# Performance work log

Measured on AMD Instinct MI355X. Metric: run time of the kernel, lower is better.

The kernel has to match this reference:

```python
import jax, jax.numpy as jnp
import numpy as np

MAX_ORDERS = 8
HIDDEN = 128
B, P = 64, 1024
FREQ_SCALE = 500.0  # Hz range for synthetic peaks
TOL = 2.0           # harmonic match tolerance from source


def setup_inputs() -> dict:
    key = jax.random.key(0)
    ks = jax.random.split(key, 6)
    peak_frequencies = jax.random.uniform(ks[0], (B, P), dtype=jnp.float32) * FREQ_SCALE
    peak_magnitudes = jax.random.normal(ks[1], (B, P), dtype=jnp.float32)
    def lin(k, fan_in, fan_out):
        return jax.random.normal(k, (fan_in, fan_out), dtype=jnp.float32) * (1.0 / np.sqrt(fan_in))
    W1 = lin(ks[2], 2, HIDDEN);        b1 = jnp.zeros((HIDDEN,), jnp.float32)
    W2 = lin(ks[3], HIDDEN, HIDDEN);   b2 = jnp.zeros((HIDDEN,), jnp.float32)
    W3 = lin(ks[4], HIDDEN, MAX_ORDERS); b3 = jnp.zeros((MAX_ORDERS,), jnp.float32)
    return {"peak_frequencies": peak_frequencies, "peak_magnitudes": peak_magnitudes,
            "W1": W1, "b1": b1, "W2": W2, "b2": b2, "W3": W3, "b3": b3}


def _fundamental_freq(freqs, mags):
    """Vectorized form of the triple-nested harmonic-matching loop.
    Returns the fundamental frequency of the LAST batch element, faithfully
    reproducing the original code (which overwrites fundamental_freq per batch)."""
    valid = mags > 0.0                                   # (B,P)
    # matched[b,i,j] = exists order in [2, max_orders] with |f_j - f_i*order| < TOL
    matched = jnp.zeros(freqs.shape[:1] + (freqs.shape[1], freqs.shape[1]), dtype=bool)
    for order in range(2, MAX_ORDERS + 1):
        matched = matched | (jnp.abs(freqs[:, None, :] - freqs[:, :, None] * order) < TOL)
    eye = jnp.eye(freqs.shape[1], dtype=bool)[None]      # exclude j == i
    harmonics = jnp.sum(matched & valid[:, None, :] & ~eye, axis=2)  # (B,P) int counts
    cand = valid & (harmonics > 0)                       # candidate peaks
    any_cand = jnp.any(cand, axis=1)                     # (B,)
    # lexicographic max over (harmonics, magnitude); argmax breaks ties by first index,
    # matching Python's stable sort over i-ascending candidate lists.
    h_masked = jnp.where(cand, harmonics, -1)
    max_h = jnp.max(h_masked, axis=1, keepdims=True)
    best = cand & (h_masked == max_h)
    mag_masked = jnp.where(best, mags, -jnp.inf)
    idx_cand = jnp.argmax(mag_masked, axis=1)
    idx_fallback = jnp.argmax(mags, axis=1)
    idx = jnp.where(any_cand, idx_cand, idx_fallback)    # (B,)
    fund = jnp.take_along_axis(freqs, idx[:, None], axis=1)[:, 0]
    return fund[-1]


def reference(peak_frequencies, peak_magnitudes, W1, b1, W2, b2, W3, b3):
    # peak_detector MLP (eval mode: dropout is identity)
    x = jnp.stack([peak_frequencies, peak_magnitudes], axis=-1)   # (B,P,2)
    h = jax.nn.relu(x @ W1 + b1)
    h = jax.nn.relu(h @ W2 + b2)
    order_probs = h @ W3 + b3                                     # (B,P,max_orders)
    fundamental_freq = _fundamental_freq(peak_frequencies, peak_magnitudes)
    return (order_probs, fundamental_freq)
```

## Files before the change

### kernel.cpp

```cpp
#include <hip/hip_runtime.h>
#include <hip/hip_bf16.h>

#define HID   128
#define PNUM  1024
#define LASTB 63
#define BP    (64 * PNUM)
#define NBLK  512
#define PPB   128
#define H2S   132

typedef __attribute__((ext_vector_type(8))) short short8;
typedef __attribute__((ext_vector_type(4))) float f32x4;

__device__ __forceinline__ unsigned pk2(float a, float b) {
    __hip_bfloat162 h = __float22bfloat162_rn(make_float2(a, b));
    union { __hip_bfloat162 h2; unsigned u; } c;
    c.h2 = h;
    return c.u;
}
__device__ __forceinline__ unsigned long long umax64(unsigned long long a,
                                                     unsigned long long b) {
    return a > b ? a : b;
}

__global__ __launch_bounds__(256) void fusedA(
    const float* __restrict__ freqs, const float* __restrict__ mags,
    const float* __restrict__ W1, const float* __restrict__ b1,
    const float* __restrict__ W2, const float* __restrict__ b2,
    const float* __restrict__ W3, const float* __restrict__ b3,
    float* __restrict__ out, unsigned long long* __restrict__ ckArr,
    unsigned long long* __restrict__ fkW)
{
    __shared__ unsigned short sW2T[HID * HID];
    __shared__ unsigned short sW3T[16 * HID];
    __shared__ float sH2[4][16 * H2S];
    __shared__ float sf[PNUM], sm[PNUM];
    __shared__ unsigned long long sfb[256];
    __shared__ unsigned long long sKey[2];
    __shared__ int sRed[4];

    const int t = threadIdx.x;
    const int b = blockIdx.x;

    {
        const float4* fb4 = reinterpret_cast<const float4*>(freqs + (size_t)LASTB * PNUM);
        const float4* mb4 = reinterpret_cast<const float4*>(mags  + (size_t)LASTB * PNUM);
        reinterpret_cast<float4*>(sf)[t] = fb4[t];
        reinterpret_cast<float4*>(sm)[t] = mb4[t];
    }

    {
        const int n    = t & 127;
        const int half = t >> 7;
#pragma unroll
        for (int r = 0; r < 8; ++r) {
            const int c  = r * 2 + half;
            const int k0 = c * 8;
            float v[8];
#pragma unroll
            for (int j = 0; j < 8; ++j) v[j] = W2[(k0 + j) * HID + n];
            union { short8 s; unsigned u[4]; } pk;
            pk.u[0] = pk2(v[0], v[1]); pk.u[1] = pk2(v[2], v[3]);
            pk.u[2] = pk2(v[4], v[5]); pk.u[3] = pk2(v[6], v[7]);
            *(short8*)&sW2T[n * HID + (c ^ (n & 15)) * 8] = pk.s;
        }
    }
    {
        const int o = t >> 4;
        const int c = t & 15;
        union { short8 s; unsigned u[4]; } pk;
        if (o < 8) {
            float v[8];
#pragma unroll
            for (int j = 0; j < 8; ++j) v[j] = W3[(c * 8 + j) * 8 + o];
            pk.u[0] = pk2(v[0], v[1]); pk.u[1] = pk2(v[2], v[3]);
            pk.u[2] = pk2(v[4], v[5]); pk.u[3] = pk2(v[6], v[7]);
        } else {
            pk.u[0] = pk.u[1] = pk.u[2] = pk.u[3] = 0u;
        }
        *(short8*)&sW3T[o * HID + (c ^ (o & 15)) * 8] = pk.s;
    }
    __syncthreads();

    {
        const int i_loc = t >> 7;
        const int jc    = t & 127;
        const int i     = b * 2 + i_loc;
        const float fi  = sf[i];
        float fo[7];
#pragma unroll
        for (int o = 0; o < 7; ++o) fo[o] = __fmul_rn(fi, (float)(o + 2));

        int c = 0;
#pragma unroll
        for (int jj = 0; jj < 8; ++jj) {
            const int j = jj * 128 + jc;
            const float fj = sf[j];
            bool match = false;
#pragma unroll
            for (int o = 0; o < 7; ++o)
                match = match || (fabsf(__fsub_rn(fj, fo[o])) < 2.0f);
            if (match && (sm[j] > 0.0f) && (j != i)) ++c;
        }
#pragma unroll
        for (int off = 32; off > 0; off >>= 1) c += __shfl_down(c, off, 64);
        if ((t & 63) == 0) sRed[t >> 6] = c;
    }
    __syncthreads();

    if ((t & 127) == 0) {
        const int i = b * 2 + (t >> 7);
        const int h = sRed[(t >> 6)] + sRed[(t >> 6) + 1];
        const float mi = sm[i];
        unsigned long long key = 0ull;
        if (mi > 0.0f && h > 0)
            key = ((unsigned long long)h << 42) |
                  ((unsigned long long)__float_as_uint(mi) << 10) |
                  (unsigned long long)(1023 - i);
        sKey[t >> 7] = key;
    }
    __syncthreads();
    if (t == 0) ckArr[b] = umax64(sKey[0], sKey[1]);

    if (b == 0) {
        unsigned long long fk = 0ull;
#pragma unroll
        for (int r = 0; r < 4; ++r) {
            const int i2 = t + 256 * r;
            const unsigned mb = __float_as_uint(sm[i2]);
            const unsigned mo = (mb & 0x80000000u) ? ~mb : (mb | 0x80000000u);
            fk = umax64(fk, ((unsigned long long)mo << 10) |
                            (unsigned long long)(1023 - i2));
        }
        sfb[t] = fk;
        __syncthreads();
        for (int s = 128; s > 0; s >>= 1) {
            if (t < s) sfb[t] = umax64(sfb[t], sfb[t + s]);
            __syncthreads();
        }
        if (t == 0) *fkW = sfb[0];
    }

    const int w    = t >> 6;
    const int lane = t & 63;
    const int cc   = lane & 15;
    const int q    = lane >> 4;
    const int pb   = b * PPB + w * 32;

    const int p0 = pb + cc;
    const int p1 = pb + 16 + cc;
    const float f0 = freqs[p0], m0 = mags[p0];
    const float f1 = freqs[p1], m1 = mags[p1];

    short8 af[2][4];
#pragma unroll
    for (int kc = 0; kc < 4; ++kc) {
        const int k0 = kc * 32 + q * 8;
        const float4 wa0 = *(const float4*)&W1[k0];
        const float4 wa1 = *(const float4*)&W1[k0 + 4];
        const float4 wb0 = *(const float4*)&W1[HID + k0];
        const float4 wb1 = *(const float4*)&W1[HID + k0 + 4];
        const float4 bb0 = *(const float4*)&b1[k0];
        const float4 bb1 = *(const float4*)&b1[k0 + 4];
        float h0[8], h1v[8];
        h0[0] = fmaxf(fmaf(f0, wa0.x, fmaf(m0, wb0.x, bb0.x)), 0.0f);
        h0[1] = fmaxf(fmaf(f0, wa0.y, fmaf(m0, wb0.y, bb0.y)), 0.0f);
        h0[2] = fmaxf(fmaf(f0, wa0.z, fmaf(m0, wb0.z, bb0.z)), 0.0f);
        h0[3] = fmaxf(fmaf(f0, wa0.w, fmaf(m0, wb0.w, bb0.w)), 0.0f);
        h0[4] = fmaxf(fmaf(f0, wa1.x, fmaf(m0, wb1.x, bb1.x)), 0.0f);
        h0[5] = fmaxf(fmaf(f0, wa1.y, fmaf(m0, wb1.y, bb1.y)), 0.0f);
        h0[6] = fmaxf(fmaf(f0, wa1.z, fmaf(m0, wb1.z, bb1.z)), 0.0f);
        h0[7] = fmaxf(fmaf(f0, wa1.w, fmaf(m0, wb1.w, bb1.w)), 0.0f);
        h1v[0] = fmaxf(fmaf(f1, wa0.x, fmaf(m1, wb0.x, bb0.x)), 0.0f);
        h1v[1] = fmaxf(fmaf(f1, wa0.y, fmaf(m1, wb0.y, bb0.y)), 0.0f);
        h1v[2] = fmaxf(fmaf(f1, wa0.z, fmaf(m1, wb0.z, bb0.z)), 0.0f);
        h1v[3] = fmaxf(fmaf(f1, wa0.w, fmaf(m1, wb0.w, bb0.w)), 0.0f);
        h1v[4] = fmaxf(fmaf(f1, wa1.x, fmaf(m1, wb1.x, bb1.x)), 0.0f);
        h1v[5] = fmaxf(fmaf(f1, wa1.y, fmaf(m1, wb1.y, bb1.y)), 0.0f);
        h1v[6] = fmaxf(fmaf(f1, wa1.z, fmaf(m1, wb1.z, bb1.z)), 0.0f);
        h1v[7] = fmaxf(fmaf(f1, wa1.w, fmaf(m1, wb1.w, bb1.w)), 0.0f);
        union { short8 s; unsigned u[4]; } u0, u1;
        u0.u[0] = pk2(h0[0], h0[1]);   u0.u[1] = pk2(h0[2], h0[3]);
        u0.u[2] = pk2(h0[4], h0[5]);   u0.u[3] = pk2(h0[6], h0[7]);
        u1.u[0] = pk2(h1v[0], h1v[1]); u1.u[1] = pk2(h1v[2], h1v[3]);
        u1.u[2] = pk2(h1v[4], h1v[5]); u1.u[3] = pk2(h1v[6], h1v[7]);
        af[0][kc] = u0.s;
        af[1][kc] = u1.s;
    }

    float b2v[8];
#pragma unroll
    for (int nt = 0; nt < 8; ++nt) b2v[nt] = b2[nt * 16 + cc];
    const float b3v = (cc < 8) ? b3[cc] : 0.0f;

    short8 bw3[4];
#pragma unroll
    for (int kc = 0; kc < 4; ++kc)
        bw3[kc] = *(const short8*)&sW3T[cc * HID + ((kc * 4 + q) ^ cc) * 8];

    f32x4 acc[2][8];
#pragma unroll
    for (int mt = 0; mt < 2; ++mt)
#pragma unroll
        for (int nt = 0; nt < 8; ++nt) {
            f32x4 z = {0.0f, 0.0f, 0.0f, 0.0f};
            acc[mt][nt] = z;
        }
#pragma unroll
    for (int nt = 0; nt < 8; ++nt)
#pragma unroll
        for (int kc = 0; kc < 4; ++kc) {
            const short8 bf = *(const short8*)
                &sW2T[(nt * 16 + cc) * HID + ((kc * 4 + q) ^ cc) * 8];
            acc[0][nt] = __builtin_amdgcn_mfma_f32_16x16x32_bf16(
                af[0][kc], bf, acc[0][nt], 0, 0, 0);
            acc[1][nt] = __builtin_amdgcn_mfma_f32_16x16x32_bf16(
                af[1][kc], bf, acc[1][nt], 0, 0, 0);
        }

    float* __restrict__ myH2 = sH2[w];
#pragma unroll
    for (int mt = 0; mt < 2; ++mt) {
#pragma unroll
        for (int nt = 0; nt < 8; ++nt) {
            const f32x4 v = acc[mt][nt];
#pragma unroll
            for (int r = 0; r < 4; ++r)
                myH2[(q * 4 + r) * H2S + nt * 16 + cc] =
                    fmaxf(v[r] + b2v[nt], 0.0f);
        }
        f32x4 oa = {0.0f, 0.0f, 0.0f, 0.0f};
#pragma unroll
        for (int kc = 0; kc < 4; ++kc) {
            const float4 x0 = *(const float4*)&myH2[cc * H2S + kc * 32 + q * 8];
            const float4 x1 = *(const float4*)&myH2[cc * H2S + kc * 32 + q * 8 + 4];
            union { short8 s; unsigned u[4]; } pk;
            pk.u[0] = pk2(x0.x, x0.y); pk.u[1] = pk2(x0.z, x0.w);
            pk.u[2] = pk2(x1.x, x1.y); pk.u[3] = pk2(x1.z, x1.w);
            oa = __builtin_amdgcn_mfma_f32_16x16x32_bf16(pk.s, bw3[kc], oa, 0, 0, 0);
        }
        if (cc < 8) {
            const int pg = pb + mt * 16 + q * 4;
#pragma unroll
            for (int r = 0; r < 4; ++r)
                out[(size_t)(pg + r) * 8 + cc] = oa[r] + b3v;
        }
    }
}

__global__ __launch_bounds__(256) void finalize(
    const float* __restrict__ freqs, const unsigned long long* __restrict__ ckArr,
    const unsigned long long* __restrict__ fkW, float* __restrict__ outF)
{
    __shared__ unsigned long long sK[256];
    const int t = threadIdx.x;
    sK[t] = umax64(ckArr[t], ckArr[t + 256]);
    __syncthreads();
    for (int s = 128; s > 0; s >>= 1) {
        if (t < s) sK[t] = umax64(sK[t], sK[t + s]);
        __syncthreads();
    }
    if (t == 0) {
        unsigned long long k = sK[0];
        if (k == 0ull) k = *fkW;
        const int idx = 1023 - (int)(k & 1023ull);
        outF[0] = freqs[(size_t)LASTB * PNUM + idx];
    }
}

extern "C" void kernel_launch(void* const* d_in, const int* in_sizes, int n_in,
                              void* d_out, int out_size, void* d_ws, size_t ws_size,
                              hipStream_t stream) {
    const float* freqs = (const float*)d_in[0];
    const float* mags  = (const float*)d_in[1];
    const float* W1    = (const float*)d_in[2];
    const float* b1    = (const float*)d_in[3];
    const float* W2    = (const float*)d_in[4];
    const float* b2    = (const float*)d_in[5];
    const float* W3    = (const float*)d_in[6];
    const float* b3    = (const float*)d_in[7];
    float* out = (float*)d_out;

    unsigned long long* ckArr = (unsigned long long*)d_ws;
    unsigned long long* fkW   = (unsigned long long*)((char*)d_ws + 4096);

    fusedA<<<NBLK, 256, 0, stream>>>(freqs, mags, W1, b1, W2, b2, W3, b3,
                                     out, ckArr, fkW);
    finalize<<<1, 256, 0, stream>>>(freqs, ckArr, fkW, out + (size_t)BP * 8);
}
```

Before: 80.08 us.

## Store H2 as bf16 in a shared scratch union to cut LDS footprint

The hidden-layer staging buffer now holds bf16 instead of fp32, so the third-layer MFMA operands are read directly as short8 with no repacking. That buffer is overlaid onto one scratch region shared with the frequency, magnitude and reduction arrays, which shrinks shared memory per block and may allow more resident blocks. The per-block key reduction is removed by writing one key per half-block to workspace, and finalize now reduces over 1024 entries. An extra barrier is added so the aliased scratch is safe to reuse.

```diff
diff --git a/kernel.cpp b/kernel.cpp
--- a/kernel.cpp
+++ b/kernel.cpp
@@ -7,11 +7,15 @@
 #define BP    (64 * PNUM)
 #define NBLK  512
 #define PPB   128
-#define H2S   132
+#define WSB   136
 
 typedef __attribute__((ext_vector_type(8))) short short8;
 typedef __attribute__((ext_vector_type(4))) float f32x4;
 
+__device__ __forceinline__ unsigned short f2bf(float x) {
+    unsigned u = __float_as_uint(x);
+    return (unsigned short)((u + 0x7FFFu + ((u >> 16) & 1u)) >> 16);
+}
 __device__ __forceinline__ unsigned pk2(float a, float b) {
     __hip_bfloat162 h = __float22bfloat162_rn(make_float2(a, b));
     union { __hip_bfloat162 h2; unsigned u; } c;
@@ -33,11 +37,13 @@
 {
     __shared__ unsigned short sW2T[HID * HID];
     __shared__ unsigned short sW3T[16 * HID];
-    __shared__ float sH2[4][16 * H2S];
-    __shared__ float sf[PNUM], sm[PNUM];
-    __shared__ unsigned long long sfb[256];
-    __shared__ unsigned long long sKey[2];
-    __shared__ int sRed[4];
+    __shared__ __align__(16) unsigned char sScr[4 * 16 * WSB * 2];
+
+    float* sf = (float*)sScr;
+    float* sm = (float*)(sScr + 4096);
+    unsigned long long* sfb = (unsigned long long*)(sScr + 8192);
+    int* sRed = (int*)(sScr + 10240);
+    unsigned short* sH2 = (unsigned short*)sScr;
 
     const int t = threadIdx.x;
     const int b = blockIdx.x;
@@ -109,7 +115,8 @@
     __syncthreads();
 
     if ((t & 127) == 0) {
-        const int i = b * 2 + (t >> 7);
+        const int half = t >> 7;
+        const int i = b * 2 + half;
         const int h = sRed[(t >> 6)] + sRed[(t >> 6) + 1];
         const float mi = sm[i];
         unsigned long long key = 0ull;
@@ -117,10 +124,8 @@
             key = ((unsigned long long)h << 42) |
                   ((unsigned long long)__float_as_uint(mi) << 10) |
                   (unsigned long long)(1023 - i);
-        sKey[t >> 7] = key;
-    }
-    __syncthreads();
-    if (t == 0) ckArr[b] = umax64(sKey[0], sKey[1]);
+        ckArr[b * 2 + half] = key;
+    }
 
     if (b == 0) {
         unsigned long long fk = 0ull;
@@ -134,12 +139,13 @@
         }
         sfb[t] = fk;
         __syncthreads();
-        for (int s = 128; s > 0; s >>= 1) {
+        for (int s = 128; s > 1; s >>= 1) {
             if (t < s) sfb[t] = umax64(sfb[t], sfb[t + s]);
             __syncthreads();
         }
-        if (t == 0) *fkW = sfb[0];
-    }
+        if (t == 0) *fkW = umax64(sfb[0], sfb[1]);
+    }
+    __syncthreads();
 
     const int w    = t >> 6;
     const int lane = t & 63;
@@ -218,7 +224,7 @@
                 af[1][kc], bf, acc[1][nt], 0, 0, 0);
         }
 
-    float* __restrict__ myH2 = sH2[w];
+    unsigned short* __restrict__ myH2 = sH2 + w * 16 * WSB;
 #pragma unroll
     for (int mt = 0; mt < 2; ++mt) {
 #pragma unroll
@@ -226,18 +232,14 @@
             const f32x4 v = acc[mt][nt];
 #pragma unroll
             for (int r = 0; r < 4; ++r)
-                myH2[(q * 4 + r) * H2S + nt * 16 + cc] =
-                    fmaxf(v[r] + b2v[nt], 0.0f);
+                myH2[(q * 4 + r) * WSB + nt * 16 + cc] =
+                    f2bf(fmaxf(v[r] + b2v[nt], 0.0f));
         }
         f32x4 oa = {0.0f, 0.0f, 0.0f, 0.0f};
 #pragma unroll
         for (int kc = 0; kc < 4; ++kc) {
-            const float4 x0 = *(const float4*)&myH2[cc * H2S + kc * 32 + q * 8];
-            const float4 x1 = *(const float4*)&myH2[cc * H2S + kc * 32 + q * 8 + 4];
-            union { short8 s; unsigned u[4]; } pk;
-            pk.u[0] = pk2(x0.x, x0.y); pk.u[1] = pk2(x0.z, x0.w);
-            pk.u[2] = pk2(x1.x, x1.y); pk.u[3] = pk2(x1.z, x1.w);
-            oa = __builtin_amdgcn_mfma_f32_16x16x32_bf16(pk.s, bw3[kc], oa, 0, 0, 0);
+            const short8 a3 = *(const short8*)&myH2[cc * WSB + kc * 32 + q * 8];
+            oa = __builtin_amdgcn_mfma_f32_16x16x32_bf16(a3, bw3[kc], oa, 0, 0, 0);
         }
         if (cc < 8) {
             const int pg = pb + mt * 16 + q * 4;
@@ -254,16 +256,19 @@
 {
     __shared__ unsigned long long sK[256];
     const int t = threadIdx.x;
-    sK[t] = umax64(ckArr[t], ckArr[t + 256]);
+    unsigned long long k = 0ull;
+#pragma unroll
+    for (int r = 0; r < 4; ++r) k = umax64(k, ckArr[t + 256 * r]);
+    sK[t] = k;
     __syncthreads();
     for (int s = 128; s > 0; s >>= 1) {
         if (t < s) sK[t] = umax64(sK[t], sK[t + s]);
         __syncthreads();
     }
     if (t == 0) {
-        unsigned long long k = sK[0];
-        if (k == 0ull) k = *fkW;
-        const int idx = 1023 - (int)(k & 1023ull);
+        unsigned long long kk = sK[0];
+        if (kk == 0ull) kk = *fkW;
+        const int idx = 1023 - (int)(kk & 1023ull);
         outF[0] = freqs[(size_t)LASTB * PNUM + idx];
     }
 }
@@ -282,7 +287,7 @@
     float* out = (float*)d_out;
 
     unsigned long long* ckArr = (unsigned long long*)d_ws;
-    unsigned long long* fkW   = (unsigned long long*)((char*)d_ws + 4096);
+    unsigned long long* fkW   = (unsigned long long*)((char*)d_ws + 8192);
 
     fusedA<<<NBLK, 256, 0, stream>>>(freqs, mags, W1, b1, W2, b2, W3, b3,
                                      out, ckArr, fkW);
```

Result: no change. 80.64 us (+0.7%).
